# Kernel optimization log

Measured on AMD Instinct MI355X. Metric: run time of the kernel, lower is better.

The kernel has to match this reference:

```python
import jax, jax.numpy as jnp
import numpy as np

EMBED_DIM = 1024
NUM_HEADS = 16
HEAD_DIM = EMBED_DIM // NUM_HEADS
SCALE = EMBED_DIM ** (-0.5)  # NOTE: module scales by embed_dim**-0.5, not head_dim**-0.5


def setup_inputs() -> dict:
    key = jax.random.key(0)
    ks = jax.random.split(key, 10)
    B, N = 2, 2048
    q = jax.random.normal(ks[0], (B, N, EMBED_DIM), dtype=jnp.float32)
    kv = jax.random.normal(ks[1], (B, N, EMBED_DIM), dtype=jnp.float32)
    mask = jax.random.randint(ks[2], (B, N), 0, 2, dtype=jnp.int64)
    s = 0.02
    Wq = jax.random.normal(ks[3], (EMBED_DIM, EMBED_DIM), dtype=jnp.float32) * s
    bq = jax.random.normal(ks[4], (EMBED_DIM,), dtype=jnp.float32) * s
    Wkv = jax.random.normal(ks[5], (EMBED_DIM, 2 * EMBED_DIM), dtype=jnp.float32) * s
    bkv = jax.random.normal(ks[6], (2 * EMBED_DIM,), dtype=jnp.float32) * s
    Wo = jax.random.normal(ks[7], (EMBED_DIM, EMBED_DIM), dtype=jnp.float32) * s
    bo = jax.random.normal(ks[8], (EMBED_DIM,), dtype=jnp.float32) * s
    return {"q": q, "kv": kv, "mask": mask, "Wq": Wq, "bq": bq,
            "Wkv": Wkv, "bkv": bkv, "Wo": Wo, "bo": bo}


def _softmax_plus_one(x):
    # softmax with +1 in the denominator; max clipped at 0, no grad through max
    m = jax.lax.stop_gradient(jnp.maximum(jnp.max(x, axis=-1, keepdims=True), 0.0))
    unnorm = jnp.exp(x - m)
    denom = jnp.sum(unnorm, axis=-1, keepdims=True) + jnp.exp(-m)
    return unnorm / denom


def _split_heads(x):
    b, n, _ = x.shape
    return x.reshape(b, n, NUM_HEADS, HEAD_DIM).transpose(0, 2, 1, 3)  # b h n d


def reference(q, kv, mask, Wq, bq, Wkv, bkv, Wo, bo):
    xq = q @ Wq + bq
    xkv = kv @ Wkv + bkv
    xk, xv = jnp.split(xkv, 2, axis=-1)
    xq, xk, xv = _split_heads(xq), _split_heads(xk), _split_heads(xv)
    logits = jnp.einsum('bhnd,bhmd->bhnm', xq * SCALE, xk)
    # prepare_mask: log of 0/1 mask broadcast over (head, query) dims
    logmask = jnp.log(mask.astype(logits.dtype))[:, None, None, :]
    logits = logits + logmask
    # attn_dropout = 0.0 -> no-op
    scores = _softmax_plus_one(logits)  # add_one_to_softmax=True
    attn = jnp.einsum('bhnm,bhmd->bhnd', scores, xv)
    b, h, n, d = attn.shape
    out = attn.transpose(0, 2, 1, 3).reshape(b, n, h * d)
    return out @ Wo + bo
```

## Files before the change

### kernel.cpp

```cpp
#include <hip/hip_runtime.h>
#include <hip/hip_bf16.h>

static constexpr int CB = 2, CN = 2048, CE = 1024, CH = 16, CD = 64;
static constexpr int CM = CB * CN;
#define SCALE_Q (1.4426950408889634f / 32.0f)

typedef __attribute__((ext_vector_type(8))) short short8;
typedef __attribute__((ext_vector_type(4))) float f32x4;
typedef __attribute__((ext_vector_type(16))) float f32x16;
typedef __attribute__((ext_vector_type(4))) float f4;
typedef __attribute__((ext_vector_type(4))) unsigned short u16x4;

#define MFMA16(a, b, c) __builtin_amdgcn_mfma_f32_16x16x32_bf16((a), (b), (c), 0, 0, 0)
#define MFMA32(a, b, c) __builtin_amdgcn_mfma_f32_32x32x16_bf16((a), (b), (c), 0, 0, 0)

static __device__ __forceinline__ unsigned short f2bf(float f) {
  union { __hip_bfloat16 h; unsigned short u; } cv;
  cv.h = __float2bfloat16(f);
  return cv.u;
}
static __device__ __forceinline__ unsigned int pk2bf(float lo, float hi) {
  return (unsigned int)f2bf(lo) | ((unsigned int)f2bf(hi) << 16);
}

typedef unsigned int u32;
static __device__ __forceinline__ void gload16(const void* g, void* l) {
  __builtin_amdgcn_global_load_lds(
      (const __attribute__((address_space(1))) u32*)g,
      (__attribute__((address_space(3))) u32*)l, 16, 0, 0);
}

#define SYNC_L()                                                 \
  do {                                                           \
    asm volatile("s_waitcnt lgkmcnt(0)" ::: "memory");           \
    __builtin_amdgcn_s_barrier();                                \
    __builtin_amdgcn_sched_barrier(0);                           \
  } while (0)

__global__ __launch_bounds__(256) void prep(
    const float* __restrict__ Wq, const float* __restrict__ Wkv,
    const float* __restrict__ Wo, unsigned short* __restrict__ WqT,
    unsigned short* __restrict__ WkvT, unsigned short* __restrict__ WoT,
    const float* __restrict__ q, const float* __restrict__ kv,
    unsigned short* __restrict__ qbf, unsigned short* __restrict__ kvbf,
    const int* __restrict__ mask, int* __restrict__ cidx, int* __restrict__ cnt) {
  __shared__ float tile[32][33];
  __shared__ int tsum[256];
  const int bid = blockIdx.x;
  const int t = threadIdx.x;
  if (bid < 4096) {
    const float* in; unsigned short* out; int C, tb;
    if (bid < 1024)      { in = Wq;  out = WqT;  C = 1024; tb = bid; }
    else if (bid < 3072) { in = Wkv; out = WkvT; C = 2048; tb = bid - 1024; }
    else                 { in = Wo;  out = WoT;  C = 1024; tb = bid - 3072; }
    const int R = 1024;
    int tc = C >> 5;
    int bc = tb % tc, br = tb / tc;
    int c = t & 31, r0 = t >> 5;
#pragma unroll
    for (int i = 0; i < 4; ++i) {
      int r = r0 + i * 8;
      tile[r][c] = in[(size_t)(br * 32 + r) * C + bc * 32 + c];
    }
    __syncthreads();
#pragma unroll
    for (int i = 0; i < 4; ++i) {
      int r = r0 + i * 8;
      out[(size_t)(bc * 32 + r) * R + br * 32 + c] = f2bf(tile[c][r]);
    }
  } else if (bid < 4098) {
    const int b = bid - 4096;
    int m[8], s = 0;
#pragma unroll
    for (int i = 0; i < 8; ++i) {
      m[i] = mask[b * CN + t * 8 + i] != 0;
      s += m[i];
    }
    tsum[t] = s;
    __syncthreads();
    if (t == 0) {
      int acc = 0;
      for (int i = 0; i < 256; ++i) { int v = tsum[i]; tsum[i] = acc; acc += v; }
      cnt[b] = acc;
    }
    __syncthreads();
    int pos = tsum[t];
#pragma unroll
    for (int i = 0; i < 8; ++i)
      if (m[i]) cidx[b * CN + pos++] = t * 8 + i;
  } else {
    const int cb = bid - 4098;
    const float* src = (cb < 2048) ? q : kv;
    unsigned short* dst = (cb < 2048) ? qbf : kvbf;
    const size_t base = (size_t)(cb & 2047) * 2048 + t * 8;
    f4 v0 = *(const f4*)(src + base);
    f4 v1 = *(const f4*)(src + base + 4);
    short8 o;
#pragma unroll
    for (int j = 0; j < 4; ++j) {
      o[j] = (short)f2bf(v0[j]);
      o[4 + j] = (short)f2bf(v1[j]);
    }
    *(short8*)(dst + base) = o;
  }
}

template <bool OUT_BF16, bool VSPLIT, bool GATHER>
static __device__ __forceinline__ void gemm_body(
    char* lds, int bm, int bn,
    const unsigned short* __restrict__ Abf, const unsigned short* __restrict__ Bt,
    const float* __restrict__ bias, void* __restrict__ C0,
    unsigned short* __restrict__ C1, int N, int K, float outscale,
    const int* __restrict__ cidx, const int* __restrict__ cnt) {
  char* As = lds;
  char* Bs = lds + 2 * 64 * 128;
  const int m0 = bm << 6, n0 = bn << 7;

  if constexpr (GATHER) {
    const int bb = m0 >> 11;
    const int ru = min((cnt[bb] + 63) & ~63, CN);
    if ((m0 & 2047) >= ru) return;
  }

  const int t = threadIdx.x;
  const int lane = t & 63, w = t >> 6;
  const int wr = w >> 1, wc = w & 1;
  const int fr = lane & 15, fg = lane >> 4;

  const int sw8 = (t & 7) ^ ((t >> 3) & 7);

  size_t arow0, arow1;
  {
    int r0 = m0 + (t >> 3), r1 = r0 + 32;
    if constexpr (GATHER) {
      const int bb = m0 >> 11;
      const int cb_ = cnt[bb];
      int c0 = (r0 & 2047), c1 = (r1 & 2047);
      c0 = c0 < cb_ ? c0 : (cb_ > 0 ? cb_ - 1 : 0);
      c1 = c1 < cb_ ? c1 : (cb_ > 0 ? cb_ - 1 : 0);
      r0 = bb * CN + cidx[bb * CN + c0];
      r1 = bb * CN + cidx[bb * CN + c1];
    }
    arow0 = (size_t)r0 * K;
    arow1 = (size_t)r1 * K;
  }

  f32x4 acc[2][4];
#pragma unroll
  for (int i = 0; i < 2; ++i)
#pragma unroll
    for (int j = 0; j < 4; ++j) acc[i][j] = (f32x4){0.f, 0.f, 0.f, 0.f};

  auto STAGE = [&](int bi, int k0) {
#pragma unroll
    for (int i = 0; i < 4; ++i) {
      int s = t + i * 256;
      gload16(Bt + (size_t)(n0 + (s >> 3)) * K + k0 + sw8 * 8,
              Bs + bi * 128 * 128 + s * 16);
    }
    gload16(Abf + arow0 + k0 + sw8 * 8, As + bi * 64 * 128 + t * 16);
    gload16(Abf + arow1 + k0 + sw8 * 8, As + bi * 64 * 128 + (t + 256) * 16);
  };

  STAGE(0, 0);
  __syncthreads();

  const int nt = K >> 6;
  int buf = 0;
  for (int tt = 0; tt < nt; ++tt) {
    const bool np = tt < nt - 1;
    if (np) STAGE(buf ^ 1, (tt + 1) << 6);
    if (np) asm volatile("s_waitcnt vmcnt(6)" ::: "memory");
    else    asm volatile("s_waitcnt vmcnt(0)" ::: "memory");
    __builtin_amdgcn_s_barrier();
    __builtin_amdgcn_sched_barrier(0);

    short8 af[2][2], bfv[4][2];
#pragma unroll
    for (int mi = 0; mi < 2; ++mi) {
      const int r = wr * 32 + mi * 16 + fr;
#pragma unroll
      for (int kk = 0; kk < 2; ++kk) {
        const int sl = (kk * 4 + fg) ^ (r & 7);
        af[mi][kk] = *(const short8*)(As + buf * 64 * 128 + r * 128 + sl * 16);
      }
    }
#pragma unroll
    for (int ni = 0; ni < 4; ++ni) {
      const int r = wc * 64 + ni * 16 + fr;
#pragma unroll
      for (int kk = 0; kk < 2; ++kk) {
        const int sl = (kk * 4 + fg) ^ (r & 7);
        bfv[ni][kk] = *(const short8*)(Bs + buf * 128 * 128 + r * 128 + sl * 16);
      }
    }
#pragma unroll
    for (int kk = 0; kk < 2; ++kk)
#pragma unroll
      for (int mi = 0; mi < 2; ++mi)
#pragma unroll
        for (int ni = 0; ni < 4; ++ni)
          acc[mi][ni] = MFMA16(af[mi][kk], bfv[ni][kk], acc[mi][ni]);

    SYNC_L();
    buf ^= 1;
  }

#pragma unroll
  for (int mi = 0; mi < 2; ++mi) {
    int row0 = m0 + wr * 32 + mi * 16 + fg * 4;
#pragma unroll
    for (int ni = 0; ni < 4; ++ni) {
      int col = n0 + wc * 64 + ni * 16 + fr;
      float bv = bias[col];
      if constexpr (VSPLIT) {
        if (col < CE) {
#pragma unroll
          for (int rr = 0; rr < 4; ++rr)
            ((unsigned short*)C0)[(size_t)(row0 + rr) * CE + col] =
                f2bf((acc[mi][ni][rr] + bv) * outscale);
        } else {
          u16x4 pk;
#pragma unroll
          for (int rr = 0; rr < 4; ++rr) pk[rr] = f2bf((acc[mi][ni][rr] + bv) * outscale);
          int b = row0 / CN, n = row0 % CN;
          *(u16x4*)&C1[((size_t)b * CE + (col - CE)) * CN + n] = pk;
        }
      } else if constexpr (OUT_BF16) {
#pragma unroll
        for (int rr = 0; rr < 4; ++rr)
          ((unsigned short*)C0)[(size_t)(row0 + rr) * N + col] =
              f2bf((acc[mi][ni][rr] + bv) * outscale);
      } else {
#pragma unroll
        for (int rr = 0; rr < 4; ++rr)
          ((float*)C0)[(size_t)(row0 + rr) * N + col] = (acc[mi][ni][rr] + bv) * outscale;
      }
    }
  }
}

__global__ __launch_bounds__(256) void gemm_qkv(
    const unsigned short* __restrict__ qbf, const unsigned short* __restrict__ WqT,
    const float* __restrict__ bq, unsigned short* __restrict__ xq,
    const unsigned short* __restrict__ kvbf, const unsigned short* __restrict__ WkvT,
    const float* __restrict__ bkv, unsigned short* __restrict__ xk,
    unsigned short* __restrict__ xvT,
    const int* __restrict__ cidx, const int* __restrict__ cnt) {
  __shared__ char lds[2 * 64 * 128 + 2 * 128 * 128];
  const int raw = blockIdx.x;
  if (raw < 512) {
    const int k = raw & 7, j = raw >> 3;
    gemm_body<true, false, false>(lds, k + 8 * (j >> 3), j & 7, qbf, WqT,
                                  bq, xq, nullptr, CE, CE, SCALE_Q,
                                  nullptr, nullptr);
  } else {
    const int r2 = raw - 512;
    const int k = r2 & 7, j = r2 >> 3;
    gemm_body<true, true, true>(lds, k + 8 * (j >> 4), j & 15, kvbf, WkvT,
                                bkv, xk, xvT, 2 * CE, CE, 1.0f, cidx, cnt);
  }
}

__global__ __launch_bounds__(256) void gemm_o(
    const unsigned short* __restrict__ attnA, const unsigned short* __restrict__ WoT,
    const float* __restrict__ bo, float* __restrict__ out) {
  __shared__ char lds[2 * 64 * 128 + 2 * 128 * 128];
  const int k = blockIdx.x & 7, j = blockIdx.x >> 3;
  gemm_body<false, false, false>(lds, k + 8 * (j >> 3), j & 7,
                                 attnA, WoT, bo, out, nullptr, CE, CE,
                                 1.0f, nullptr, nullptr);
}

__global__ __launch_bounds__(256, 2) void attn_fwd(
    unsigned short* __restrict__ xq,
    const unsigned short* __restrict__ xk,
    const unsigned short* __restrict__ xvT,
    const int* __restrict__ cnt) {
  __shared__ unsigned short Kt[64][72];
  __shared__ unsigned short Vt[64][72];
  __shared__ float dsh[4][32];

  const int bid = blockIdx.x;
  const int qblk = bid & 15;
  const int h = (bid >> 4) & 15;
  const int b = bid >> 8;
  const int t = threadIdx.x, lane = t & 63, w = t >> 6;
  const int l31 = lane & 31, h5 = lane >> 5;
  const int q0 = qblk * 128 + w * 32;

  const int cntb = cnt[b];
  const int nt = (cntb + 63) >> 6;

  short8 qf[4];
  {
    const unsigned short* qp =
        xq + ((size_t)(b * CN + q0 + l31)) * CE + h * CD + h5 * 8;
#pragma unroll
    for (int dk = 0; dk < 4; ++dk) qf[dk] = *(const short8*)(qp + dk * 16);
  }

  f32x16 o[2];
#pragma unroll
  for (int c = 0; c < 2; ++c)
#pragma unroll
    for (int i = 0; i < 16; ++i) o[c][i] = 0.f;
  float ls = 0.f;

  const int r0s = t >> 3, sl0 = t & 7;
  const int r1s = r0s + 32, sl1 = sl0;

  short8 rk[2], rv[2];
  if (nt > 0) {
    rk[0] = *(const short8*)(xk + ((size_t)(b * CN + r0s)) * CE + h * CD + sl0 * 8);
    rk[1] = *(const short8*)(xk + ((size_t)(b * CN + r1s)) * CE + h * CD + sl1 * 8);
    rv[0] = *(const short8*)(xvT + ((size_t)(b * CE + h * CD + r0s)) * CN + sl0 * 8);
    rv[1] = *(const short8*)(xvT + ((size_t)(b * CE + h * CD + r1s)) * CN + sl1 * 8);
  }

  for (int kt = 0; kt < nt; ++kt) {
    __syncthreads();
    *(short8*)&Kt[r0s][sl0 * 8] = rk[0];
    *(short8*)&Kt[r1s][sl1 * 8] = rk[1];
    *(short8*)&Vt[r0s][sl0 * 8] = rv[0];
    *(short8*)&Vt[r1s][sl1 * 8] = rv[1];
    __syncthreads();

    if (kt < nt - 1) {
      const int kn = (kt + 1) * 64;
      rk[0] = *(const short8*)(xk + ((size_t)(b * CN + kn + r0s)) * CE + h * CD + sl0 * 8);
      rk[1] = *(const short8*)(xk + ((size_t)(b * CN + kn + r1s)) * CE + h * CD + sl1 * 8);
      rv[0] = *(const short8*)(xvT + ((size_t)(b * CE + h * CD + r0s)) * CN + kn + sl0 * 8);
      rv[1] = *(const short8*)(xvT + ((size_t)(b * CE + h * CD + r1s)) * CN + kn + sl1 * 8);
    }

    short8 ka[2][4];
#pragma unroll
    for (int cb = 0; cb < 2; ++cb)
#pragma unroll
      for (int dk = 0; dk < 4; ++dk)
        ka[cb][dk] = *(const short8*)&Kt[cb * 32 + l31][(dk * 2 + h5) * 8];

    f32x16 s2[2];
#pragma unroll
    for (int cb = 0; cb < 2; ++cb) {
#pragma unroll
      for (int i = 0; i < 16; ++i) s2[cb][i] = 0.f;
#pragma unroll
      for (int dk = 0; dk < 4; ++dk)
        s2[cb] = MFMA32(ka[cb][dk], qf[dk], s2[cb]);
    }

    const bool tail = (kt == nt - 1) && (cntb & 63);
    unsigned int U[2][4][2];
#pragma unroll
    for (int cb = 0; cb < 2; ++cb) {
      float p[16];
#pragma unroll
      for (int i = 0; i < 16; ++i) {
        float sv = s2[cb][i];
        if (tail) {
          int cpos = kt * 64 + cb * 32 + (i & 3) + 8 * (i >> 2) + 4 * h5;
          sv = (cpos < cntb) ? sv : -30000.f;
        }
        p[i] = __builtin_amdgcn_exp2f(sv);
        ls += p[i];
      }
#pragma unroll
      for (int m = 0; m < 4; ++m) {
        U[cb][m][0] = pk2bf(p[4 * m], p[4 * m + 1]);
        U[cb][m][1] = pk2bf(p[4 * m + 2], p[4 * m + 3]);
      }
    }

    short8 vb[2][4];
#pragma unroll
    for (int nb = 0; nb < 2; ++nb)
#pragma unroll
      for (int kc = 0; kc < 4; ++kc)
        vb[nb][kc] = *(const short8*)&Vt[nb * 32 + l31][(kc * 2 + h5) * 8];

#pragma unroll
    for (int kc = 0; kc < 4; ++kc) {
      const int cb = kc >> 1, k2 = (kc & 1) * 2;
      unsigned int su0 = h5 ? U[cb][k2 + 1][0] : U[cb][k2][0];
      unsigned int su1 = h5 ? U[cb][k2 + 1][1] : U[cb][k2][1];
      unsigned int st0 = h5 ? U[cb][k2][0] : U[cb][k2 + 1][0];
      unsigned int st1 = h5 ? U[cb][k2][1] : U[cb][k2 + 1][1];
      unsigned int x0 = (unsigned int)__shfl_xor((int)st0, 32);
      unsigned int x1 = (unsigned int)__shfl_xor((int)st1, 32);
      union { unsigned int u[4]; short8 v; } pa;
      pa.u[0] = h5 ? x0 : su0;
      pa.u[1] = h5 ? x1 : su1;
      pa.u[2] = h5 ? su0 : x0;
      pa.u[3] = h5 ? su1 : x1;
#pragma unroll
      for (int nb = 0; nb < 2; ++nb)
        o[nb] = MFMA32(pa.v, vb[nb][kc], o[nb]);
    }
  }

  {
    float tot = ls + __shfl_xor(ls, 32);
    if (h5 == 0) dsh[w][l31] = 1.0f / (tot + 1.0f);
  }
  __syncthreads();
#pragma unroll
  for (int m = 0; m < 4; ++m) {
    f4 dn4 = *(const f4*)&dsh[w][m * 8 + h5 * 4];
#pragma unroll
    for (int rr = 0; rr < 4; ++rr) {
      int q = m * 8 + h5 * 4 + rr;
      size_t row = (size_t)(b * CN + q0 + q);
#pragma unroll
      for (int nb = 0; nb < 2; ++nb) {
        float val = o[nb][m * 4 + rr] * dn4[rr];
        xq[row * CE + h * CD + nb * 32 + l31] = f2bf(val);
      }
    }
  }
}

extern "C" void kernel_launch(void* const* d_in, const int* in_sizes, int n_in,
                              void* d_out, int out_size, void* d_ws, size_t ws_size,
                              hipStream_t stream) {
  const float* q    = (const float*)d_in[0];
  const float* kv   = (const float*)d_in[1];
  const int*   mask = (const int*)d_in[2];
  const float* Wq   = (const float*)d_in[3];
  const float* bq   = (const float*)d_in[4];
  const float* Wkv  = (const float*)d_in[5];
  const float* bkv  = (const float*)d_in[6];
  const float* Wo   = (const float*)d_in[7];
  const float* bo   = (const float*)d_in[8];
  (void)in_sizes; (void)n_in; (void)out_size; (void)ws_size;

  char* ws = (char*)d_ws;
  unsigned short* WoT  = (unsigned short*)(ws);
  unsigned short* xq   = (unsigned short*)(ws + (2u  << 20));
  unsigned short* xk   = (unsigned short*)(ws + (10u << 20));
  unsigned short* xvT  = (unsigned short*)(ws + (18u << 20));
  unsigned short* WqT  = (unsigned short*)(ws + (26u << 20));
  unsigned short* WkvT = (unsigned short*)(ws + (28u << 20));
  unsigned short* qbf  = (unsigned short*)(ws + (32u << 20));
  unsigned short* kvbf = (unsigned short*)(ws + (40u << 20));
  int*            cidx = (int*)(ws + (48u << 20));
  int*            cnt  = (int*)(ws + (48u << 20) + 16384);

  prep<<<8194, 256, 0, stream>>>(Wq, Wkv, Wo, WqT, WkvT, WoT,
                                 q, kv, qbf, kvbf, mask, cidx, cnt);

  gemm_qkv<<<1536, 256, 0, stream>>>(qbf, WqT, bq, xq, kvbf, WkvT, bkv,
                                     xk, xvT, cidx, cnt);

  attn_fwd<<<CB * CH * 16, 256, 0, stream>>>(xq, xk, xvT, cnt);

  gemm_o<<<512, 256, 0, stream>>>(xq, WoT, bo, (float*)d_out);
}
```

Measured before the change: 88.72 us.

## Halve attention block to 2 waves, double grid, add MFMA setprio

The attention kernel now runs 128-thread blocks that each cover 64 query rows instead of 256 threads covering 128, and the grid doubles to 1024 blocks. Each thread loads four K/V rows per tile instead of two to keep tile staging intact. s_setprio raises wave priority around the MFMA sections. The aim is better load balance and CU fill across 256 CUs, at the cost of each K/V tile being fetched from global memory twice as often per query.

Result: slower. 93.65 us (+5.6%).

```diff
diff --git a/kernel.cpp b/kernel.cpp
--- a/kernel.cpp
+++ b/kernel.cpp
@@ -272,22 +272,22 @@
                                  1.0f, nullptr, nullptr);
 }
 
-__global__ __launch_bounds__(256, 2) void attn_fwd(
+__global__ __launch_bounds__(128, 2) void attn_fwd(
     unsigned short* __restrict__ xq,
     const unsigned short* __restrict__ xk,
     const unsigned short* __restrict__ xvT,
     const int* __restrict__ cnt) {
   __shared__ unsigned short Kt[64][72];
   __shared__ unsigned short Vt[64][72];
-  __shared__ float dsh[4][32];
+  __shared__ float dsh[2][32];
 
   const int bid = blockIdx.x;
-  const int qblk = bid & 15;
-  const int h = (bid >> 4) & 15;
-  const int b = bid >> 8;
+  const int qblk = bid & 31;
+  const int h = (bid >> 5) & 15;
+  const int b = bid >> 9;
   const int t = threadIdx.x, lane = t & 63, w = t >> 6;
   const int l31 = lane & 31, h5 = lane >> 5;
-  const int q0 = qblk * 128 + w * 32;
+  const int q0 = qblk * 64 + w * 32;
 
   const int cntb = cnt[b];
   const int nt = (cntb + 63) >> 6;
@@ -307,31 +307,33 @@
     for (int i = 0; i < 16; ++i) o[c][i] = 0.f;
   float ls = 0.f;
 
-  const int r0s = t >> 3, sl0 = t & 7;
-  const int r1s = r0s + 32, sl1 = sl0;
-
-  short8 rk[2], rv[2];
+  const int rs = t >> 3, sl = t & 7;
+
+  short8 rk[4], rv[4];
   if (nt > 0) {
-    rk[0] = *(const short8*)(xk + ((size_t)(b * CN + r0s)) * CE + h * CD + sl0 * 8);
-    rk[1] = *(const short8*)(xk + ((size_t)(b * CN + r1s)) * CE + h * CD + sl1 * 8);
-    rv[0] = *(const short8*)(xvT + ((size_t)(b * CE + h * CD + r0s)) * CN + sl0 * 8);
-    rv[1] = *(const short8*)(xvT + ((size_t)(b * CE + h * CD + r1s)) * CN + sl1 * 8);
+#pragma unroll
+    for (int p = 0; p < 4; ++p) {
+      rk[p] = *(const short8*)(xk + ((size_t)(b * CN + rs + p * 16)) * CE + h * CD + sl * 8);
+      rv[p] = *(const short8*)(xvT + ((size_t)(b * CE + h * CD + rs + p * 16)) * CN + sl * 8);
+    }
   }
 
   for (int kt = 0; kt < nt; ++kt) {
     __syncthreads();
-    *(short8*)&Kt[r0s][sl0 * 8] = rk[0];
-    *(short8*)&Kt[r1s][sl1 * 8] = rk[1];
-    *(short8*)&Vt[r0s][sl0 * 8] = rv[0];
-    *(short8*)&Vt[r1s][sl1 * 8] = rv[1];
+#pragma unroll
+    for (int p = 0; p < 4; ++p) {
+      *(short8*)&Kt[rs + p * 16][sl * 8] = rk[p];
+      *(short8*)&Vt[rs + p * 16][sl * 8] = rv[p];
+    }
     __syncthreads();
 
     if (kt < nt - 1) {
       const int kn = (kt + 1) * 64;
-      rk[0] = *(const short8*)(xk + ((size_t)(b * CN + kn + r0s)) * CE + h * CD + sl0 * 8);
-      rk[1] = *(const short8*)(xk + ((size_t)(b * CN + kn + r1s)) * CE + h * CD + sl1 * 8);
-      rv[0] = *(const short8*)(xvT + ((size_t)(b * CE + h * CD + r0s)) * CN + kn + sl0 * 8);
-      rv[1] = *(const short8*)(xvT + ((size_t)(b * CE + h * CD + r1s)) * CN + kn + sl1 * 8);
+#pragma unroll
+      for (int p = 0; p < 4; ++p) {
+        rk[p] = *(const short8*)(xk + ((size_t)(b * CN + kn + rs + p * 16)) * CE + h * CD + sl * 8);
+        rv[p] = *(const short8*)(xvT + ((size_t)(b * CE + h * CD + rs + p * 16)) * CN + kn + sl * 8);
+      }
     }
 
     short8 ka[2][4];
@@ -342,6 +344,7 @@
         ka[cb][dk] = *(const short8*)&Kt[cb * 32 + l31][(dk * 2 + h5) * 8];
 
     f32x16 s2[2];
+    __builtin_amdgcn_s_setprio(1);
 #pragma unroll
     for (int cb = 0; cb < 2; ++cb) {
 #pragma unroll
@@ -350,6 +353,7 @@
       for (int dk = 0; dk < 4; ++dk)
         s2[cb] = MFMA32(ka[cb][dk], qf[dk], s2[cb]);
     }
+    __builtin_amdgcn_s_setprio(0);
 
     const bool tail = (kt == nt - 1) && (cntb & 63);
     unsigned int U[2][4][2];
@@ -380,6 +384,7 @@
       for (int kc = 0; kc < 4; ++kc)
         vb[nb][kc] = *(const short8*)&Vt[nb * 32 + l31][(kc * 2 + h5) * 8];
 
+    __builtin_amdgcn_s_setprio(1);
 #pragma unroll
     for (int kc = 0; kc < 4; ++kc) {
       const int cb = kc >> 1, k2 = (kc & 1) * 2;
@@ -398,6 +403,7 @@
       for (int nb = 0; nb < 2; ++nb)
         o[nb] = MFMA32(pa.v, vb[nb][kc], o[nb]);
     }
+    __builtin_amdgcn_s_setprio(0);
   }
 
   {
@@ -453,7 +459,7 @@
   gemm_qkv<<<1536, 256, 0, stream>>>(qbf, WqT, bq, xq, kvbf, WkvT, bkv,
                                      xk, xvT, cidx, cnt);
 
-  attn_fwd<<<CB * CH * 16, 256, 0, stream>>>(xq, xk, xvT, cnt);
+  attn_fwd<<<CB * CH * 32, 128, 0, stream>>>(xq, xk, xvT, cnt);
 
   gemm_o<<<512, 256, 0, stream>>>(xq, WoT, bo, (float*)d_out);
 }
```
